# Kernel tuning notes

Hardware: AMD Instinct MI355X
Metric: run time of the kernel (lower is better)

## Reference

```python
import jax, jax.numpy as jnp
import numpy as np

N_EMBED = 384
BLOCK_SIZE = 256
HEAD_SIZE = 64
B, T = 256, 256


def setup_inputs() -> dict:
    key = jax.random.key(0)
    k1, k2, k3, k4 = jax.random.split(key, 4)
    x = jax.random.normal(k1, (B, T, N_EMBED), dtype=jnp.float32)
    Wq = jax.random.normal(k2, (N_EMBED, HEAD_SIZE), dtype=jnp.float32) * (N_EMBED ** -0.5)
    Wk = jax.random.normal(k3, (N_EMBED, HEAD_SIZE), dtype=jnp.float32) * (N_EMBED ** -0.5)
    Wv = jax.random.normal(k4, (N_EMBED, HEAD_SIZE), dtype=jnp.float32) * (N_EMBED ** -0.5)
    return {"x": x, "Wq": Wq, "Wk": Wk, "Wv": Wv}


def reference(x, Wq, Wk, Wv):
    Bb, Tt, C = x.shape
    q = jnp.einsum("btc,ch->bth", x, Wq)
    k = jnp.einsum("btc,ch->bth", x, Wk)
    v = jnp.einsum("btc,ch->bth", x, Wv)
    # NOTE: original scales by C**-0.5 where C = n_embed (384), not head_size
    scale = jnp.asarray(C, x.dtype) ** -0.5
    wei = jnp.einsum("bqh,bkh->bqk", q, k) * scale  # [B, T, T]
    causal = jnp.tril(jnp.ones((Tt, Tt), dtype=bool))
    wei = jnp.where(causal, wei, -jnp.inf)
    wei = jax.nn.softmax(wei, axis=-1)
    out = jnp.einsum("bqk,bkh->bqh", wei, v)
    return out
```

## Files before the change

### kernel.cpp

```cpp
#include <hip/hip_runtime.h>
#include <hip/hip_bf16.h>
#include <math.h>

#define BB   256
#define TT   256
#define CIN  384
#define HS   64
#define BT   (BB*TT)

#define QSCL ((float)(0.051031036307982884 * 1.4426950408889634))

typedef __attribute__((ext_vector_type(8))) short short8;
typedef __attribute__((ext_vector_type(4))) float floatx4;

__device__ inline short bf16bits(float f) {
    union { __hip_bfloat16 h; short s; } u;
    u.h = __float2bfloat16(f);
    return u.s;
}

__device__ inline short8 cvt8(const float4& f0, const float4& f1) {
    union { __hip_bfloat162 h[4]; short8 s8; } u;
    u.h[0] = __float22bfloat162_rn(make_float2(f0.x, f0.y));
    u.h[1] = __float22bfloat162_rn(make_float2(f0.z, f0.w));
    u.h[2] = __float22bfloat162_rn(make_float2(f1.x, f1.y));
    u.h[3] = __float22bfloat162_rn(make_float2(f1.z, f1.w));
    return u.s8;
}

__global__ __launch_bounds__(256) void prep_wt(
    const float* __restrict__ Wq, const float* __restrict__ Wk,
    const float* __restrict__ Wv, short* __restrict__ Wt)
{
    const int idx = blockIdx.x * 256 + threadIdx.x;
    const int n  = idx / 384;
    const int kk = idx - n * 384;
    const float* W = (n < 64) ? Wq : (n < 128) ? Wk : Wv;
    Wt[idx] = bf16bits(W[kk * 64 + (n & 63)]);
}

__global__ __launch_bounds__(256) void qkv_mfma(
    const float* __restrict__ x, const short* __restrict__ Wt,
    short* __restrict__ q, short* __restrict__ k, short* __restrict__ vT)
{
    __shared__ short smem[27136];

    const int tid  = threadIdx.x;
    const int lane = tid & 63;
    const int w    = tid >> 6;
    const int wm   = w >> 1;
    const int wn   = w & 1;
    const int l15  = lane & 15;
    const int quad = lane >> 4;
    const int kq   = quad * 8;
    const int crow = quad * 4;

    const int mbase0 = blockIdx.x * 128;
    const int nbase  = wn * 96;

    floatx4 acc[4][6] = {};

    const short* wp[6];
#pragma unroll
    for (int nt = 0; nt < 6; ++nt)
        wp[nt] = Wt + (size_t)(nbase + nt * 16 + l15) * 384 + kq;

#pragma unroll
    for (int i = 0; i < 4; ++i) {
        const int c   = i * 256 + tid;
        const int row = c >> 3;
        const int ch  = (c & 7) * 8;
        const float* p = x + (size_t)(mbase0 + row) * 384 + ch;
        *(short8*)&smem[row * 72 + ch] = cvt8(*(const float4*)p, *(const float4*)(p + 4));
    }
    __syncthreads();

#pragma unroll
    for (int s = 0; s < 6; ++s) {
        short* cur = smem + (s & 1) * 9216;
        short* nxt = smem + ((s & 1) ^ 1) * 9216;

        short8 bf[2][6];
#pragma unroll
        for (int nt = 0; nt < 6; ++nt) {
            bf[0][nt] = *(const short8*)(wp[nt] + s * 64);
            bf[1][nt] = *(const short8*)(wp[nt] + s * 64 + 32);
        }

        float4 pf[4][2];
        if (s < 5) {
#pragma unroll
            for (int i = 0; i < 4; ++i) {
                const int c   = i * 256 + tid;
                const int row = c >> 3;
                const int ch  = (c & 7) * 8;
                const float* p = x + (size_t)(mbase0 + row) * 384 + (s + 1) * 64 + ch;
                pf[i][0] = *(const float4*)p;
                pf[i][1] = *(const float4*)(p + 4);
            }
        }

#pragma unroll
        for (int ks = 0; ks < 2; ++ks) {
            short8 af[4];
#pragma unroll
            for (int mt = 0; mt < 4; ++mt)
                af[mt] = *(const short8*)&cur[(wm * 64 + mt * 16 + l15) * 72 + ks * 32 + kq];
#pragma unroll
            for (int mt = 0; mt < 4; ++mt)
#pragma unroll
                for (int nt = 0; nt < 6; ++nt)
                    acc[mt][nt] = __builtin_amdgcn_mfma_f32_16x16x32_bf16(
                        af[mt], bf[ks][nt], acc[mt][nt], 0, 0, 0);
        }

        if (s < 5) {
#pragma unroll
            for (int i = 0; i < 4; ++i) {
                const int c   = i * 256 + tid;
                const int row = c >> 3;
                const int ch  = (c & 7) * 8;
                *(short8*)&nxt[row * 72 + ch] = cvt8(pf[i][0], pf[i][1]);
            }
        }
        __syncthreads();
    }

    short (*q_lds)[72]   = (short(*)[72])  smem;
    short (*k_lds)[72]   = (short(*)[72]) (smem + 9216);
    short (*vt_lds)[136] = (short(*)[136])(smem + 18432);

#pragma unroll
    for (int nt = 0; nt < 6; ++nt) {
        const int n = nbase + nt * 16 + l15;
#pragma unroll
        for (int mt = 0; mt < 4; ++mt) {
#pragma unroll
            for (int r = 0; r < 4; ++r) {
                const int m = wm * 64 + mt * 16 + crow + r;
                const float av = acc[mt][nt][r];
                if (n < 64)       q_lds[m][n]        = bf16bits(av * QSCL);
                else if (n < 128) k_lds[m][n - 64]   = bf16bits(av);
                else              vt_lds[n - 128][m] = bf16bits(av);
            }
        }
    }
    __syncthreads();

    const int b  = blockIdx.x >> 1;
    const int t0 = (blockIdx.x & 1) * 128;
#pragma unroll
    for (int i = 0; i < 4; ++i) {
        const int c = i * 256 + tid;
        {
            const int row = c >> 3;
            const int c8  = (c & 7) * 8;
            *(short8*)&q[(size_t)(mbase0 + row) * 64 + c8] = *(const short8*)&q_lds[row][c8];
            *(short8*)&k[(size_t)(mbase0 + row) * 64 + c8] = *(const short8*)&k_lds[row][c8];
        }
        {
            const int h  = c >> 4;
            const int t8 = (c & 15) * 8;
            *(short8*)&vT[(size_t)(b * 64 + h) * 256 + t0 + t8] = *(const short8*)&vt_lds[h][t8];
        }
    }
}

__global__ __launch_bounds__(256) void attn_mfma(
    const short* __restrict__ q,
    const short* __restrict__ k,
    const short* __restrict__ vT,
    float* __restrict__ out)
{
    __shared__ short Ks[128][72];
    __shared__ short Vt[64][136];
    __shared__ short Ps[4][16][40];

    const int tid  = threadIdx.x;
    const int b    = blockIdx.x >> 2;
    const int qt   = blockIdx.x & 3;
    const int lane = tid & 63;
    const int w    = tid >> 6;
    const int l15  = lane & 15;
    const int quad = lane >> 4;
    const int kq   = quad * 8;
    const int crow = quad * 4;

    const int q0g  = qt * 64 + w * 16;
    const int kmax = q0g + 16;

    short8 aq[2];
    {
        const short* qp = q + (size_t)(b * 256 + q0g + l15) * 64;
        aq[0] = *(const short8*)(qp + kq);
        aq[1] = *(const short8*)(qp + 32 + kq);
    }

    float lsum[4] = {0.f, 0.f, 0.f, 0.f};
    floatx4 O[4] = {};

    const int nstages = (qt >= 2) ? 2 : 1;
    for (int s = 0; s < nstages; ++s) {
        if (s) __syncthreads();
        const int sbase = s * 128;

#pragma unroll
        for (int i = 0; i < 4; ++i) {
            const int c   = i * 256 + tid;
            const int key = c >> 3;
            const int c8  = (c & 7) * 8;
            *(short8*)&Ks[key][c8] =
                *(const short8*)(k + (size_t)(b * 256 + sbase + key) * 64 + c8);
        }
#pragma unroll
        for (int i = 0; i < 4; ++i) {
            const int c  = i * 256 + tid;
            const int h  = c >> 4;
            const int t8 = (c & 15) * 8;
            *(short8*)&Vt[h][t8] =
                *(const short8*)(vT + (size_t)(b * 64 + h) * 256 + sbase + t8);
        }
        __syncthreads();

        const int rem = kmax - sbase;
        const int nch = rem >= 128 ? 4 : ((rem + 31) >> 5);
        for (int c = 0; c < nch; ++c) {
            const int cb = c * 32;

            floatx4 st[2];
#pragma unroll
            for (int t = 0; t < 2; ++t) {
                const short8 b0 = *(const short8*)&Ks[cb + t * 16 + l15][kq];
                const short8 b1 = *(const short8*)&Ks[cb + t * 16 + l15][32 + kq];
                floatx4 z = {};
                z = __builtin_amdgcn_mfma_f32_16x16x32_bf16(aq[0], b0, z, 0, 0, 0);
                z = __builtin_amdgcn_mfma_f32_16x16x32_bf16(aq[1], b1, z, 0, 0, 0);
                st[t] = z;
            }

#pragma unroll
            for (int t = 0; t < 2; ++t)
#pragma unroll
                for (int r = 0; r < 4; ++r) {
                    const int key  = sbase + cb + t * 16 + l15;
                    const int qrow = q0g + crow + r;
                    float p = __builtin_amdgcn_exp2f(st[t][r]);
                    p = (key <= qrow) ? p : 0.f;
                    lsum[r] += p;
                    Ps[w][crow + r][t * 16 + l15] = bf16bits(p);
                }

            asm volatile("s_waitcnt lgkmcnt(0)" ::: "memory");

            const short8 pa = *(const short8*)&Ps[w][l15][kq];
#pragma unroll
            for (int n = 0; n < 4; ++n) {
                const short8 bv = *(const short8*)&Vt[n * 16 + l15][cb + kq];
                O[n] = __builtin_amdgcn_mfma_f32_16x16x32_bf16(pa, bv, O[n], 0, 0, 0);
            }
        }
    }

#pragma unroll
    for (int off = 1; off < 16; off <<= 1)
#pragma unroll
        for (int r = 0; r < 4; ++r)
            lsum[r] += __shfl_xor(lsum[r], off, 16);

    float inv[4];
#pragma unroll
    for (int r = 0; r < 4; ++r) inv[r] = 1.f / lsum[r];
#pragma unroll
    for (int n = 0; n < 4; ++n)
#pragma unroll
        for (int r = 0; r < 4; ++r)
            out[(size_t)(b * 256 + q0g + crow + r) * 64 + n * 16 + l15] = O[n][r] * inv[r];
}

extern "C" void kernel_launch(void* const* d_in, const int* in_sizes, int n_in,
                              void* d_out, int out_size, void* d_ws, size_t ws_size,
                              hipStream_t stream)
{
    const float* x  = (const float*)d_in[0];
    const float* Wq = (const float*)d_in[1];
    const float* Wk = (const float*)d_in[2];
    const float* Wv = (const float*)d_in[3];
    float* out = (float*)d_out;

    short* Wt = (short*)d_ws;
    short* qb = (short*)((char*)d_ws + 256 * 1024);
    short* kb = qb + (size_t)BT * HS;
    short* vT = kb + (size_t)BT * HS;

    prep_wt<<<(192 * 384) / 256, 256, 0, stream>>>(Wq, Wk, Wv, Wt);
    qkv_mfma<<<BT / 128, 256, 0, stream>>>(x, Wt, qb, kb, vT);
    attn_mfma<<<BB * 4, 256, 0, stream>>>(qb, kb, vT, out);
}
```

Measured before the change: 189.4 us.

## Fuse QKV projection and causal attention into one per-batch kernel

Adds a 512-thread kernel that handles one batch per block. It computes Q, K and V^T with MFMA, holds them in LDS, and runs causal attention in place, so the intermediate q/k/vT never round-trip through global memory and one launch disappears. The cost is grid parallelism: only 256 blocks with about 115KB of LDS each, which limits occupancy. Softmax skips the max-subtraction, and the old two-kernel path is kept as a fallback when the launch errors.

```diff
diff --git a/kernel.cpp b/kernel.cpp
--- a/kernel.cpp
+++ b/kernel.cpp
@@ -39,6 +39,181 @@
     Wt[idx] = bf16bits(W[kk * 64 + (n & 63)]);
 }
 
+__global__ __launch_bounds__(512) void fused_head(
+    const float* __restrict__ x, const short* __restrict__ Wt,
+    float* __restrict__ out)
+{
+    __shared__ short smem[58880];
+
+    const int tid  = threadIdx.x;
+    const int b    = blockIdx.x;
+    const int lane = tid & 63;
+    const int w    = tid >> 6;
+    const int wm   = w >> 1;
+    const int wn   = w & 1;
+    const int l15  = lane & 15;
+    const int quad = lane >> 4;
+    const int kq   = quad * 8;
+    const int crow = quad * 4;
+
+    const int nbase = wn * 96;
+    const float* xb = x + (size_t)b * 256 * 384;
+
+    floatx4 acc[4][6] = {};
+
+    const short* wp[6];
+#pragma unroll
+    for (int nt = 0; nt < 6; ++nt)
+        wp[nt] = Wt + (size_t)(nbase + nt * 16 + l15) * 384 + kq;
+
+#pragma unroll
+    for (int i = 0; i < 4; ++i) {
+        const int c   = i * 512 + tid;
+        const int row = c >> 3;
+        const int ch  = (c & 7) * 8;
+        const float* p = xb + (size_t)row * 384 + ch;
+        *(short8*)&smem[row * 72 + ch] = cvt8(*(const float4*)p, *(const float4*)(p + 4));
+    }
+    __syncthreads();
+
+#pragma unroll
+    for (int s = 0; s < 6; ++s) {
+        short* cur = smem + (s & 1) * 18432;
+        short* nxt = smem + ((s & 1) ^ 1) * 18432;
+
+        short8 bf[2][6];
+#pragma unroll
+        for (int nt = 0; nt < 6; ++nt) {
+            bf[0][nt] = *(const short8*)(wp[nt] + s * 64);
+            bf[1][nt] = *(const short8*)(wp[nt] + s * 64 + 32);
+        }
+
+        float4 pf[4][2];
+        if (s < 5) {
+#pragma unroll
+            for (int i = 0; i < 4; ++i) {
+                const int c   = i * 512 + tid;
+                const int row = c >> 3;
+                const int ch  = (c & 7) * 8;
+                const float* p = xb + (size_t)row * 384 + (s + 1) * 64 + ch;
+                pf[i][0] = *(const float4*)p;
+                pf[i][1] = *(const float4*)(p + 4);
+            }
+        }
+
+#pragma unroll
+        for (int ks = 0; ks < 2; ++ks) {
+            short8 af[4];
+#pragma unroll
+            for (int mt = 0; mt < 4; ++mt)
+                af[mt] = *(const short8*)&cur[(wm * 64 + mt * 16 + l15) * 72 + ks * 32 + kq];
+#pragma unroll
+            for (int mt = 0; mt < 4; ++mt)
+#pragma unroll
+                for (int nt = 0; nt < 6; ++nt)
+                    acc[mt][nt] = __builtin_amdgcn_mfma_f32_16x16x32_bf16(
+                        af[mt], bf[ks][nt], acc[mt][nt], 0, 0, 0);
+        }
+
+        if (s < 5) {
+#pragma unroll
+            for (int i = 0; i < 4; ++i) {
+                const int c   = i * 512 + tid;
+                const int row = c >> 3;
+                const int ch  = (c & 7) * 8;
+                *(short8*)&nxt[row * 72 + ch] = cvt8(pf[i][0], pf[i][1]);
+            }
+        }
+        __syncthreads();
+    }
+
+    short* q_lds = smem;
+    short* k_lds = smem + 18432;
+    short* vt    = smem + 36864;
+    short* Ps    = smem + 53760;
+
+#pragma unroll
+    for (int nt = 0; nt < 6; ++nt) {
+        const int n = nbase + nt * 16 + l15;
+#pragma unroll
+        for (int mt = 0; mt < 4; ++mt) {
+#pragma unroll
+            for (int r = 0; r < 4; ++r) {
+                const int m = wm * 64 + mt * 16 + crow + r;
+                const float av = acc[mt][nt][r];
+                if (n < 64)       q_lds[m * 72 + n]          = bf16bits(av * QSCL);
+                else if (n < 128) k_lds[m * 72 + (n - 64)]   = bf16bits(av);
+                else              vt[(n - 128) * 264 + m]    = bf16bits(av);
+            }
+        }
+    }
+    __syncthreads();
+
+#pragma unroll
+    for (int g = 0; g < 2; ++g) {
+        const int r0 = w * 32 + g * 16;
+
+        short8 aq0, aq1;
+        aq0 = *(const short8*)&q_lds[(r0 + l15) * 72 + kq];
+        aq1 = *(const short8*)&q_lds[(r0 + l15) * 72 + 32 + kq];
+
+        float lsum[4] = {0.f, 0.f, 0.f, 0.f};
+        floatx4 O[4] = {};
+
+        const int nch = (r0 + 47) >> 5;
+        for (int c = 0; c < nch; ++c) {
+            const int cb = c * 32;
+
+            floatx4 st[2];
+#pragma unroll
+            for (int t = 0; t < 2; ++t) {
+                const short8 b0 = *(const short8*)&k_lds[(cb + t * 16 + l15) * 72 + kq];
+                const short8 b1 = *(const short8*)&k_lds[(cb + t * 16 + l15) * 72 + 32 + kq];
+                floatx4 z = {};
+                z = __builtin_amdgcn_mfma_f32_16x16x32_bf16(aq0, b0, z, 0, 0, 0);
+                z = __builtin_amdgcn_mfma_f32_16x16x32_bf16(aq1, b1, z, 0, 0, 0);
+                st[t] = z;
+            }
+
+#pragma unroll
+            for (int t = 0; t < 2; ++t)
+#pragma unroll
+                for (int r = 0; r < 4; ++r) {
+                    const int key  = cb + t * 16 + l15;
+                    const int qrow = r0 + crow + r;
+                    float p = __builtin_amdgcn_exp2f(st[t][r]);
+                    p = (key <= qrow) ? p : 0.f;
+                    lsum[r] += p;
+                    Ps[w * 640 + (crow + r) * 40 + t * 16 + l15] = bf16bits(p);
+                }
+
+            asm volatile("s_waitcnt lgkmcnt(0)" ::: "memory");
+
+            const short8 pa = *(const short8*)&Ps[w * 640 + l15 * 40 + kq];
+#pragma unroll
+            for (int n = 0; n < 4; ++n) {
+                const short8 bv = *(const short8*)&vt[(n * 16 + l15) * 264 + cb + kq];
+                O[n] = __builtin_amdgcn_mfma_f32_16x16x32_bf16(pa, bv, O[n], 0, 0, 0);
+            }
+        }
+
+#pragma unroll
+        for (int off = 1; off < 16; off <<= 1)
+#pragma unroll
+            for (int r = 0; r < 4; ++r)
+                lsum[r] += __shfl_xor(lsum[r], off, 16);
+
+        float inv[4];
+#pragma unroll
+        for (int r = 0; r < 4; ++r) inv[r] = 1.f / lsum[r];
+#pragma unroll
+        for (int n = 0; n < 4; ++n)
+#pragma unroll
+            for (int r = 0; r < 4; ++r)
+                out[(size_t)(b * 256 + r0 + crow + r) * 64 + n * 16 + l15] = O[n][r] * inv[r];
+    }
+}
+
 __global__ __launch_bounds__(256) void qkv_mfma(
     const float* __restrict__ x, const short* __restrict__ Wt,
     short* __restrict__ q, short* __restrict__ k, short* __restrict__ vT)
@@ -147,7 +322,7 @@
     }
     __syncthreads();
 
-    const int b  = blockIdx.x >> 1;
+    const int bb = blockIdx.x >> 1;
     const int t0 = (blockIdx.x & 1) * 128;
 #pragma unroll
     for (int i = 0; i < 4; ++i) {
@@ -161,7 +336,7 @@
         {
             const int h  = c >> 4;
             const int t8 = (c & 15) * 8;
-            *(short8*)&vT[(size_t)(b * 64 + h) * 256 + t0 + t8] = *(const short8*)&vt_lds[h][t8];
+            *(short8*)&vT[(size_t)(bb * 64 + h) * 256 + t0 + t8] = *(const short8*)&vt_lds[h][t8];
         }
     }
 }
@@ -293,6 +468,10 @@
     short* vT = kb + (size_t)BT * HS;
 
     prep_wt<<<(192 * 384) / 256, 256, 0, stream>>>(Wq, Wk, Wv, Wt);
-    qkv_mfma<<<BT / 128, 256, 0, stream>>>(x, Wt, qb, kb, vT);
-    attn_mfma<<<BB * 4, 256, 0, stream>>>(qb, kb, vT, out);
-}
+
+    fused_head<<<BB, 512, 0, stream>>>(x, Wt, out);
+    if (hipGetLastError() != hipSuccess) {
+        qkv_mfma<<<BT / 128, 256, 0, stream>>>(x, Wt, qb, kb, vT);
+        attn_mfma<<<BB * 4, 256, 0, stream>>>(qb, kb, vT, out);
+    }
+}
```

After: 181.8 us. -4.1%, faster.

## Fuse QKV projection and causal attention into one per-batch kernel

Applied to the files above, without the earlier changes.

Merges the QKV projection and the attention kernel into one 512-thread block per batch element. Q, K and V^T stay in LDS instead of going through global memory. The weights are pre-permuted into the MFMA fragment order so each lane loads contiguous values, and the x loads are double-buffered two stages ahead. This removes the global round trip for q/k/v and one kernel launch. In exchange it uses much more LDS per block, launches only 256 blocks, and gives waves uneven causal work, which hurts occupancy and load balance.

```diff
diff --git a/kernel.cpp b/kernel.cpp
--- a/kernel.cpp
+++ b/kernel.cpp
@@ -28,24 +28,34 @@
     return u.s8;
 }
 
-__global__ __launch_bounds__(256) void prep_wt(
+__global__ __launch_bounds__(256) void prep_wtp(
     const float* __restrict__ Wq, const float* __restrict__ Wk,
-    const float* __restrict__ Wv, short* __restrict__ Wt)
+    const float* __restrict__ Wv, short* __restrict__ WtP)
 {
-    const int idx = blockIdx.x * 256 + threadIdx.x;
-    const int n  = idx / 384;
-    const int kk = idx - n * 384;
+    const int idx  = blockIdx.x * 256 + threadIdx.x;
+    const int j    = idx & 7;
+    const int quad = (idx >> 3) & 3;
+    const int l15  = (idx >> 5) & 15;
+    int X          = idx >> 9;
+    const int nt   = X % 6;  X /= 6;
+    const int ks   = X & 1;  X >>= 1;
+    const int s    = X % 6;  X /= 6;
+    const int wn   = X;
+
+    const int n  = wn * 96 + nt * 16 + l15;
+    const int kk = s * 64 + ks * 32 + quad * 8 + j;
     const float* W = (n < 64) ? Wq : (n < 128) ? Wk : Wv;
-    Wt[idx] = bf16bits(W[kk * 64 + (n & 63)]);
-}
-
-__global__ __launch_bounds__(256) void qkv_mfma(
-    const float* __restrict__ x, const short* __restrict__ Wt,
-    short* __restrict__ q, short* __restrict__ k, short* __restrict__ vT)
+    WtP[idx] = bf16bits(W[kk * 64 + (n & 63)]);
+}
+
+__global__ __launch_bounds__(512) void fused_head(
+    const float* __restrict__ x, const short* __restrict__ WtP,
+    float* __restrict__ out)
 {
-    __shared__ short smem[27136];
+    __shared__ short smem[58880];
 
     const int tid  = threadIdx.x;
+    const int b    = blockIdx.x;
     const int lane = tid & 63;
     const int w    = tid >> 6;
     const int wm   = w >> 1;
@@ -55,50 +65,55 @@
     const int kq   = quad * 8;
     const int crow = quad * 4;
 
-    const int mbase0 = blockIdx.x * 128;
-    const int nbase  = wn * 96;
+    const float* xb = x + (size_t)b * 256 * 384;
+    const int laneoff = l15 * 32 + quad * 8;
 
     floatx4 acc[4][6] = {};
 
-    const short* wp[6];
-#pragma unroll
-    for (int nt = 0; nt < 6; ++nt)
-        wp[nt] = Wt + (size_t)(nbase + nt * 16 + l15) * 384 + kq;
-
 #pragma unroll
     for (int i = 0; i < 4; ++i) {
-        const int c   = i * 256 + tid;
+        const int c   = i * 512 + tid;
         const int row = c >> 3;
         const int ch  = (c & 7) * 8;
-        const float* p = x + (size_t)(mbase0 + row) * 384 + ch;
+        const float* p = xb + (size_t)row * 384 + ch;
         *(short8*)&smem[row * 72 + ch] = cvt8(*(const float4*)p, *(const float4*)(p + 4));
     }
+    float4 pf[2][4][2];
+#pragma unroll
+    for (int i = 0; i < 4; ++i) {
+        const int c   = i * 512 + tid;
+        const int row = c >> 3;
+        const int ch  = (c & 7) * 8;
+        const float* p = xb + (size_t)row * 384 + 64 + ch;
+        pf[1][i][0] = *(const float4*)p;
+        pf[1][i][1] = *(const float4*)(p + 4);
+    }
     __syncthreads();
 
 #pragma unroll
     for (int s = 0; s < 6; ++s) {
-        short* cur = smem + (s & 1) * 9216;
-        short* nxt = smem + ((s & 1) ^ 1) * 9216;
-
-        short8 bf[2][6];
-#pragma unroll
-        for (int nt = 0; nt < 6; ++nt) {
-            bf[0][nt] = *(const short8*)(wp[nt] + s * 64);
-            bf[1][nt] = *(const short8*)(wp[nt] + s * 64 + 32);
-        }
-
-        float4 pf[4][2];
-        if (s < 5) {
+        short* cur = smem + (s & 1) * 18432;
+        short* nxt = smem + ((s & 1) ^ 1) * 18432;
+
+        if (s < 4) {
 #pragma unroll
             for (int i = 0; i < 4; ++i) {
-                const int c   = i * 256 + tid;
+                const int c   = i * 512 + tid;
                 const int row = c >> 3;
                 const int ch  = (c & 7) * 8;
-                const float* p = x + (size_t)(mbase0 + row) * 384 + (s + 1) * 64 + ch;
-                pf[i][0] = *(const float4*)p;
-                pf[i][1] = *(const float4*)(p + 4);
-            }
-        }
+                const float* p = xb + (size_t)row * 384 + (s + 2) * 64 + ch;
+                pf[s & 1][i][0] = *(const float4*)p;
+                pf[s & 1][i][1] = *(const float4*)(p + 4);
+            }
+        }
+
+        short8 bf[2][6];
+#pragma unroll
+        for (int ks = 0; ks < 2; ++ks)
+#pragma unroll
+            for (int nt = 0; nt < 6; ++nt)
+                bf[ks][nt] = *(const short8*)
+                    &WtP[((((wn * 6 + s) * 2 + ks) * 6 + nt) << 9) + laneoff];
 
 #pragma unroll
         for (int ks = 0; ks < 2; ++ks) {
@@ -117,19 +132,22 @@
         if (s < 5) {
 #pragma unroll
             for (int i = 0; i < 4; ++i) {
-                const int c   = i * 256 + tid;
+                const int c   = i * 512 + tid;
                 const int row = c >> 3;
                 const int ch  = (c & 7) * 8;
-                *(short8*)&nxt[row * 72 + ch] = cvt8(pf[i][0], pf[i][1]);
+                *(short8*)&nxt[row * 72 + ch] =
+                    cvt8(pf[(s + 1) & 1][i][0], pf[(s + 1) & 1][i][1]);
             }
         }
         __syncthreads();
     }
 
-    short (*q_lds)[72]   = (short(*)[72])  smem;
-    short (*k_lds)[72]   = (short(*)[72]) (smem + 9216);
-    short (*vt_lds)[136] = (short(*)[136])(smem + 18432);
-
+    short* q_lds = smem;
+    short* k_lds = smem + 18432;
+    short* vt    = smem + 36864;
+    short* Ps    = smem + 53760;
+
+    const int nbase = wn * 96;
 #pragma unroll
     for (int nt = 0; nt < 6; ++nt) {
         const int n = nbase + nt * 16 + l15;
@@ -139,102 +157,37 @@
             for (int r = 0; r < 4; ++r) {
                 const int m = wm * 64 + mt * 16 + crow + r;
                 const float av = acc[mt][nt][r];
-                if (n < 64)       q_lds[m][n]        = bf16bits(av * QSCL);
-                else if (n < 128) k_lds[m][n - 64]   = bf16bits(av);
-                else              vt_lds[n - 128][m] = bf16bits(av);
+                if (n < 64)       q_lds[m * 72 + n]          = bf16bits(av * QSCL);
+                else if (n < 128) k_lds[m * 72 + (n - 64)]   = bf16bits(av);
+                else              vt[(n - 128) * 264 + m]    = bf16bits(av);
             }
         }
     }
     __syncthreads();
 
-    const int b  = blockIdx.x >> 1;
-    const int t0 = (blockIdx.x & 1) * 128;
-#pragma unroll
-    for (int i = 0; i < 4; ++i) {
-        const int c = i * 256 + tid;
-        {
-            const int row = c >> 3;
-            const int c8  = (c & 7) * 8;
-            *(short8*)&q[(size_t)(mbase0 + row) * 64 + c8] = *(const short8*)&q_lds[row][c8];
-            *(short8*)&k[(size_t)(mbase0 + row) * 64 + c8] = *(const short8*)&k_lds[row][c8];
-        }
-        {
-            const int h  = c >> 4;
-            const int t8 = (c & 15) * 8;
-            *(short8*)&vT[(size_t)(b * 64 + h) * 256 + t0 + t8] = *(const short8*)&vt_lds[h][t8];
-        }
-    }
-}
-
-__global__ __launch_bounds__(256) void attn_mfma(
-    const short* __restrict__ q,
-    const short* __restrict__ k,
-    const short* __restrict__ vT,
-    float* __restrict__ out)
-{
-    __shared__ short Ks[128][72];
-    __shared__ short Vt[64][136];
-    __shared__ short Ps[4][16][40];
-
-    const int tid  = threadIdx.x;
-    const int b    = blockIdx.x >> 2;
-    const int qt   = blockIdx.x & 3;
-    const int lane = tid & 63;
-    const int w    = tid >> 6;
-    const int l15  = lane & 15;
-    const int quad = lane >> 4;
-    const int kq   = quad * 8;
-    const int crow = quad * 4;
-
-    const int q0g  = qt * 64 + w * 16;
-    const int kmax = q0g + 16;
-
-    short8 aq[2];
-    {
-        const short* qp = q + (size_t)(b * 256 + q0g + l15) * 64;
-        aq[0] = *(const short8*)(qp + kq);
-        aq[1] = *(const short8*)(qp + 32 + kq);
-    }
-
-    float lsum[4] = {0.f, 0.f, 0.f, 0.f};
-    floatx4 O[4] = {};
-
-    const int nstages = (qt >= 2) ? 2 : 1;
-    for (int s = 0; s < nstages; ++s) {
-        if (s) __syncthreads();
-        const int sbase = s * 128;
-
-#pragma unroll
-        for (int i = 0; i < 4; ++i) {
-            const int c   = i * 256 + tid;
-            const int key = c >> 3;
-            const int c8  = (c & 7) * 8;
-            *(short8*)&Ks[key][c8] =
-                *(const short8*)(k + (size_t)(b * 256 + sbase + key) * 64 + c8);
-        }
-#pragma unroll
-        for (int i = 0; i < 4; ++i) {
-            const int c  = i * 256 + tid;
-            const int h  = c >> 4;
-            const int t8 = (c & 15) * 8;
-            *(short8*)&Vt[h][t8] =
-                *(const short8*)(vT + (size_t)(b * 64 + h) * 256 + sbase + t8);
-        }
-        __syncthreads();
-
-        const int rem = kmax - sbase;
-        const int nch = rem >= 128 ? 4 : ((rem + 31) >> 5);
+#pragma unroll
+    for (int g = 0; g < 2; ++g) {
+        const int r0 = w * 32 + g * 16;
+
+        short8 aq0, aq1;
+        aq0 = *(const short8*)&q_lds[(r0 + l15) * 72 + kq];
+        aq1 = *(const short8*)&q_lds[(r0 + l15) * 72 + 32 + kq];
+
+        float lsum[4] = {0.f, 0.f, 0.f, 0.f};
+        floatx4 O[4] = {};
+
+        const int nch = (r0 + 47) >> 5;
         for (int c = 0; c < nch; ++c) {
             const int cb = c * 32;
 
             floatx4 st[2];
 #pragma unroll
             for (int t = 0; t < 2; ++t) {
-                const short8 b0 = *(const short8*)&Ks[cb + t * 16 + l15][kq];
-                const short8 b1 = *(const short8*)&Ks[cb + t * 16 + l15][32 + kq];
+                const short8 b0 = *(const short8*)&k_lds[(cb + t * 16 + l15) * 72 + kq];
+                const short8 b1 = *(const short8*)&k_lds[(cb + t * 16 + l15) * 72 + 32 + kq];
                 floatx4 z = {};
-                z = __builtin_amdgcn_mfma_f32_16x16x32_bf16(aq[0], b0, z, 0, 0, 0);
-                z = __builtin_amdgcn_mfma_f32_16x16x32_bf16(aq[1], b1, z, 0, 0, 0);
+                z = __builtin_amdgcn_mfma_f32_16x16x32_bf16(aq0, b0, z, 0, 0, 0);
+                z = __builtin_amdgcn_mfma_f32_16x16x32_bf16(aq1, b1, z, 0, 0, 0);
                 st[t] = z;
             }
 
@@ -242,39 +195,39 @@
             for (int t = 0; t < 2; ++t)
 #pragma unroll
                 for (int r = 0; r < 4; ++r) {
-                    const int key  = sbase + cb + t * 16 + l15;
-                    const int qrow = q0g + crow + r;
+                    const int key  = cb + t * 16 + l15;
+                    const int qrow = r0 + crow + r;
                     float p = __builtin_amdgcn_exp2f(st[t][r]);
                     p = (key <= qrow) ? p : 0.f;
                     lsum[r] += p;
-                    Ps[w][crow + r][t * 16 + l15] = bf16bits(p);
+                    Ps[w * 640 + (crow + r) * 40 + t * 16 + l15] = bf16bits(p);
                 }
 
             asm volatile("s_waitcnt lgkmcnt(0)" ::: "memory");
 
-            const short8 pa = *(const short8*)&Ps[w][l15][kq];
+            const short8 pa = *(const short8*)&Ps[w * 640 + l15 * 40 + kq];
 #pragma unroll
             for (int n = 0; n < 4; ++n) {
-                const short8 bv = *(const short8*)&Vt[n * 16 + l15][cb + kq];
+                const short8 bv = *(const short8*)&vt[(n * 16 + l15) * 264 + cb + kq];
                 O[n] = __builtin_amdgcn_mfma_f32_16x16x32_bf16(pa, bv, O[n], 0, 0, 0);
             }
         }
-    }
-
-#pragma unroll
-    for (int off = 1; off < 16; off <<= 1)
-#pragma unroll
-        for (int r = 0; r < 4; ++r)
-            lsum[r] += __shfl_xor(lsum[r], off, 16);
-
-    float inv[4];
-#pragma unroll
-    for (int r = 0; r < 4; ++r) inv[r] = 1.f / lsum[r];
-#pragma unroll
-    for (int n = 0; n < 4; ++n)
-#pragma unroll
-        for (int r = 0; r < 4; ++r)
-            out[(size_t)(b * 256 + q0g + crow + r) * 64 + n * 16 + l15] = O[n][r] * inv[r];
+
+#pragma unroll
+        for (int off = 1; off < 16; off <<= 1)
+#pragma unroll
+            for (int r = 0; r < 4; ++r)
+                lsum[r] += __shfl_xor(lsum[r], off, 16);
+
+        float inv[4];
+#pragma unroll
+        for (int r = 0; r < 4; ++r) inv[r] = 1.f / lsum[r];
+#pragma unroll
+        for (int n = 0; n < 4; ++n)
+#pragma unroll
+            for (int r = 0; r < 4; ++r)
+                out[(size_t)(b * 256 + r0 + crow + r) * 64 + n * 16 + l15] = O[n][r] * inv[r];
+    }
 }
 
 extern "C" void kernel_launch(void* const* d_in, const int* in_sizes, int n_in,
@@ -287,12 +240,8 @@
     const float* Wv = (const float*)d_in[3];
     float* out = (float*)d_out;
 
-    short* Wt = (short*)d_ws;
-    short* qb = (short*)((char*)d_ws + 256 * 1024);
-    short* kb = qb + (size_t)BT * HS;
-    short* vT = kb + (size_t)BT * HS;
-
-    prep_wt<<<(192 * 384) / 256, 256, 0, stream>>>(Wq, Wk, Wv, Wt);
-    qkv_mfma<<<BT / 128, 256, 0, stream>>>(x, Wt, qb, kb, vT);
-    attn_mfma<<<BB * 4, 256, 0, stream>>>(qb, kb, vT, out);
-}
+    short* WtP = (short*)d_ws;
+
+    prep_wtp<<<(192 * 384) / 256, 256, 0, stream>>>(Wq, Wk, Wv, WtP);
+    fused_head<<<BB, 512, 0, stream>>>(x, WtP, out);
+}
```

Measured after the change: 172.1 us. 9.2% less time.
